# Performance work log

Measured on AMD Instinct MI355X. Metric: run time of the kernel, lower is better.

Reference implementation:

```python
import jax, jax.numpy as jnp
import numpy as np

HIDDEN = 2048
NUM_HEADS = 16
HEAD_DIM = HIDDEN // NUM_HEADS  # 128
SCALE = HEAD_DIM ** -0.5


def setup_inputs() -> dict:
    key = jax.random.key(0)
    ks = jax.random.split(key, 5)
    B, S = 2, 2048
    init = HIDDEN ** -0.5  # roughly kaiming-uniform scale for Linear weights
    return {
        "hidden_states": jax.random.normal(ks[0], (B, S, HIDDEN), dtype=jnp.float32),
        "Wq": jax.random.normal(ks[1], (HIDDEN, HIDDEN), dtype=jnp.float32) * init,
        "Wk": jax.random.normal(ks[2], (HIDDEN, HIDDEN), dtype=jnp.float32) * init,
        "Wv": jax.random.normal(ks[3], (HIDDEN, HIDDEN), dtype=jnp.float32) * init,
        "Wo": jax.random.normal(ks[4], (HIDDEN, HIDDEN), dtype=jnp.float32) * init,
    }


def reference(hidden_states, Wq, Wk, Wv, Wo):
    B, S, _ = hidden_states.shape
    # Projections (nn.Linear: x @ W.T; weights stored as [out, in])
    q = (hidden_states @ Wq.T).reshape(B, S, NUM_HEADS, HEAD_DIM).transpose(0, 2, 1, 3)
    k = (hidden_states @ Wk.T).reshape(B, S, NUM_HEADS, HEAD_DIM).transpose(0, 2, 1, 3)
    v = (hidden_states @ Wv.T).reshape(B, S, NUM_HEADS, HEAD_DIM).transpose(0, 2, 1, 3)
    # Full quadratic attention (faithful to the source's explicit materialization)
    scores = jnp.einsum("bhqd,bhkd->bhqk", q, k) * SCALE  # [B,H,S,S]
    probs = jax.nn.softmax(scores, axis=-1)
    attn = jnp.einsum("bhqk,bhkd->bhqd", probs, v)  # [B,H,S,Dh]
    attn = attn.transpose(0, 2, 1, 3).reshape(B, S, HIDDEN)
    return attn @ Wo.T
```

## Files before the change

kernel.cpp:

```cpp
#include <hip/hip_runtime.h>
#include <cstdint>

#define HIDDEN 2048
#define NHEADS 16
#define DH 128
#define BATCH 2
#define SEQ 2048
#define MTOT 4096
#define BH (BATCH * NHEADS)

typedef __attribute__((ext_vector_type(8))) short bf16x8;
typedef __attribute__((ext_vector_type(4))) float f32x4;

static constexpr float QSCALE = (float)(0.08838834764831845 * 1.4426950408889634);

__device__ __forceinline__ unsigned short f2bf(float f) {
  union { float f; uint32_t u; } v; v.f = f;
  uint32_t r = v.u + 0x7FFFu + ((v.u >> 16) & 1u);
  return (unsigned short)(r >> 16);
}
__device__ __forceinline__ uint32_t cvtpk(float lo, float hi) {
  uint32_t r;
  asm("v_cvt_pk_bf16_f32 %0, %1, %2" : "=v"(r) : "v"(lo), "v"(hi));
  return r;
}
__device__ __forceinline__ f32x4 mfma16(bf16x8 a, bf16x8 b, f32x4 c) {
  return __builtin_amdgcn_mfma_f32_16x16x32_bf16(a, b, c, 0, 0, 0);
}

typedef const __attribute__((address_space(1))) unsigned char* gas1_t;
typedef __attribute__((address_space(3))) unsigned char* las3_t;
__device__ __forceinline__ void gll16(const void* g, void* l) {
  __builtin_amdgcn_global_load_lds((gas1_t)g, (las3_t)l, 16, 0, 0);
}

__global__ __launch_bounds__(256) void cast_all(
    const float* __restrict__ X, const float* __restrict__ Wq,
    const float* __restrict__ Wk, const float* __restrict__ Wv,
    const float* __restrict__ Wo, unsigned short* __restrict__ Xb,
    unsigned short* __restrict__ Wqb, unsigned short* __restrict__ Wkb,
    unsigned short* __restrict__ Wvb, unsigned short* __restrict__ Wob) {
  const int n1 = MTOT * HIDDEN;
  const int i = (blockIdx.x * 256 + threadIdx.x) * 4;
  const float* s;
  unsigned short* d;
  int o;
  if (i < n1) {
    s = X; d = Xb; o = i;
  } else {
    const int j = i - n1;
    const int w = j >> 22;
    o = j & ((1 << 22) - 1);
    s = (w == 0) ? Wq : (w == 1) ? Wk : (w == 2) ? Wv : Wo;
    d = (w == 0) ? Wqb : (w == 1) ? Wkb : (w == 2) ? Wvb : Wob;
  }
  float4 f = *(const float4*)&s[o];
  ushort4 u;
  u.x = f2bf(f.x); u.y = f2bf(f.y); u.z = f2bf(f.z); u.w = f2bf(f.w);
  *(ushort4*)&d[o] = u;
}

template <int VM, bool PF>
__device__ __forceinline__ void pipe_body(
    int kt, char* SM, const unsigned short* aS0, const unsigned short* aS1,
    const unsigned short* bS0, const unsigned short* bS1,
    const unsigned short* bS2, const unsigned short* bS3, int wv, int wr,
    int wc, int g, int lr, f32x4 (&acc)[4][4]) {
  const char* Ac = SM + (kt % 3) * 49152;
  const char* Bc = Ac + 16384;
  char* slot2 = SM + ((kt + 2) % 3) * 49152;
  const size_t ko = (size_t)(kt + 2) * 64;
  const int rx = lr & 7;
  bf16x8 a0[4], b0[4], a1[4], b1[4];
#pragma unroll
  for (int mi = 0; mi < 4; ++mi)
    a0[mi] = *(const bf16x8*)(Ac + (wr * 64 + mi * 16 + lr) * 128 + ((g ^ rx) * 16));
#pragma unroll
  for (int ni = 0; ni < 4; ++ni)
    b0[ni] = *(const bf16x8*)(Bc + (wc * 64 + ni * 16 + lr) * 128 + ((g ^ rx) * 16));
  if (PF) {
    gll16(aS0 + ko, slot2 + wv * 2048);
    gll16(aS1 + ko, slot2 + wv * 2048 + 1024);
    gll16(bS0 + ko, slot2 + 16384 + wv * 4096);
    gll16(bS1 + ko, slot2 + 16384 + wv * 4096 + 1024);
    gll16(bS2 + ko, slot2 + 16384 + wv * 4096 + 2048);
    gll16(bS3 + ko, slot2 + 16384 + wv * 4096 + 3072);
  }
#pragma unroll
  for (int mi = 0; mi < 4; ++mi)
    a1[mi] = *(const bf16x8*)(Ac + (wr * 64 + mi * 16 + lr) * 128 + (((4 + g) ^ rx) * 16));
#pragma unroll
  for (int ni = 0; ni < 4; ++ni)
    b1[ni] = *(const bf16x8*)(Bc + (wc * 64 + ni * 16 + lr) * 128 + (((4 + g) ^ rx) * 16));
  __builtin_amdgcn_s_setprio(1);
#pragma unroll
  for (int mi = 0; mi < 4; ++mi)
#pragma unroll
    for (int ni = 0; ni < 4; ++ni)
      acc[mi][ni] = mfma16(a0[mi], b0[ni], acc[mi][ni]);
#pragma unroll
  for (int mi = 0; mi < 4; ++mi)
#pragma unroll
    for (int ni = 0; ni < 4; ++ni)
      acc[mi][ni] = mfma16(a1[mi], b1[ni], acc[mi][ni]);
  __builtin_amdgcn_s_setprio(0);
  if (VM == 6) asm volatile("s_waitcnt vmcnt(6)" ::: "memory");
  else if (VM == 0) asm volatile("s_waitcnt vmcnt(0)" ::: "memory");
  if (VM >= 0) __builtin_amdgcn_s_barrier();
}

#define PIPE_SETUP(Abase, Bbase)                                              \
  const int idxA0 = wv * 128 + lane, idxA1 = idxA0 + 64;                      \
  const int rA0 = idxA0 >> 3, cA0 = (idxA0 & 7) ^ (rA0 & 7);                  \
  const int rA1 = idxA1 >> 3, cA1 = (idxA1 & 7) ^ (rA1 & 7);                  \
  const unsigned short* aS0 = (Abase) + (size_t)(m0 + rA0) * HIDDEN + cA0 * 8;\
  const unsigned short* aS1 = (Abase) + (size_t)(m0 + rA1) * HIDDEN + cA1 * 8;\
  const int idxB0 = wv * 256 + lane, idxB1 = idxB0 + 64,                      \
            idxB2 = idxB0 + 128, idxB3 = idxB0 + 192;                         \
  const int rB0 = idxB0 >> 3, cB0 = (idxB0 & 7) ^ (rB0 & 7);                  \
  const int rB1 = idxB1 >> 3, cB1 = (idxB1 & 7) ^ (rB1 & 7);                  \
  const int rB2 = idxB2 >> 3, cB2 = (idxB2 & 7) ^ (rB2 & 7);                  \
  const int rB3 = idxB3 >> 3, cB3 = (idxB3 & 7) ^ (rB3 & 7);                  \
  const unsigned short* bS0 = (Bbase) + (size_t)(n0 + rB0) * HIDDEN + cB0 * 8;\
  const unsigned short* bS1 = (Bbase) + (size_t)(n0 + rB1) * HIDDEN + cB1 * 8;\
  const unsigned short* bS2 = (Bbase) + (size_t)(n0 + rB2) * HIDDEN + cB2 * 8;\
  const unsigned short* bS3 = (Bbase) + (size_t)(n0 + rB3) * HIDDEN + cB3 * 8;

#define PIPE_PROLOGUE()                                                       \
  _Pragma("unroll") for (int tt = 0; tt < 2; ++tt) {                          \
    char* slot = SM + tt * 49152;                                             \
    const size_t ko = (size_t)tt * 64;                                        \
    gll16(aS0 + ko, slot + wv * 2048);                                        \
    gll16(aS1 + ko, slot + wv * 2048 + 1024);                                 \
    gll16(bS0 + ko, slot + 16384 + wv * 4096);                                \
    gll16(bS1 + ko, slot + 16384 + wv * 4096 + 1024);                         \
    gll16(bS2 + ko, slot + 16384 + wv * 4096 + 2048);                         \
    gll16(bS3 + ko, slot + 16384 + wv * 4096 + 3072);                         \
  }                                                                           \
  asm volatile("s_waitcnt vmcnt(6)" ::: "memory");                            \
  __builtin_amdgcn_s_barrier();

#define PIPE_LOOP()                                                           \
  for (int kt = 0; kt < 30; ++kt)                                             \
    pipe_body<6, true>(kt, SM, aS0, aS1, bS0, bS1, bS2, bS3, wv, wr, wc, g,   \
                       lr, acc);                                              \
  pipe_body<0, false>(30, SM, aS0, aS1, bS0, bS1, bS2, bS3, wv, wr, wc, g,    \
                      lr, acc);                                               \
  pipe_body<-1, false>(31, SM, aS0, aS1, bS0, bS1, bS2, bS3, wv, wr, wc, g,   \
                       lr, acc);

__global__ __launch_bounds__(512) void gemm_qkv_pipe(
    const unsigned short* __restrict__ A, const unsigned short* __restrict__ Wq,
    const unsigned short* __restrict__ Wk, const unsigned short* __restrict__ Wv,
    unsigned short* __restrict__ Qb, unsigned short* __restrict__ Kb,
    unsigned short* __restrict__ Vb) {
  __shared__ __align__(16) char SM[147456];
  const int tid = threadIdx.x;
  const int lane = tid & 63, wv = tid >> 6;
  const int wr = wv >> 2, wc = wv & 3;
  const int g = lane >> 4, lr = lane & 15;
  const int which = blockIdx.x >> 3;
  const int m0 = blockIdx.y * 128, n0 = (blockIdx.x & 7) * 256;
  const unsigned short* W = (which == 0) ? Wq : (which == 1) ? Wk : Wv;

  PIPE_SETUP(A, W)

  f32x4 acc[4][4];
#pragma unroll
  for (int i = 0; i < 4; ++i)
#pragma unroll
    for (int j = 0; j < 4; ++j) acc[i][j] = (f32x4){0.f, 0.f, 0.f, 0.f};

  PIPE_PROLOGUE()
  PIPE_LOOP()

  const float alpha = (which == 0) ? QSCALE : 1.0f;
  unsigned short* C = (which == 0) ? Qb : (which == 1) ? Kb : Vb;
#pragma unroll
  for (int mi = 0; mi < 4; ++mi)
#pragma unroll
    for (int ni = 0; ni < 4; ++ni)
#pragma unroll
      for (int r = 0; r < 4; ++r) {
        const int row = m0 + wr * 64 + mi * 16 + g * 4 + r;
        const int col = n0 + wc * 64 + ni * 16 + lr;
        const unsigned short v = f2bf(acc[mi][ni][r] * alpha);
        const int b = row >> 11, s = row & (SEQ - 1);
        const int h = col >> 7, d = col & (DH - 1);
        const size_t base = (size_t)(b * NHEADS + h) * SEQ * DH;
        if (which == 0)
          C[base + (size_t)s * DH + d] = v;
        else if (which == 1)
          C[base + (size_t)(s >> 5) * 4096 + (d >> 3) * 256 + (s & 31) * 8 + (d & 7)] = v;
        else
          C[base + (size_t)(s >> 3) * 1024 + d * 8 + (s & 7)] = v;
      }
}

__global__ __launch_bounds__(512) void gemm_out_pipe(
    const unsigned short* __restrict__ A, const unsigned short* __restrict__ W,
    float* __restrict__ C) {
  __shared__ __align__(16) char SM[147456];
  const int tid = threadIdx.x;
  const int lane = tid & 63, wv = tid >> 6;
  const int wr = wv >> 2, wc = wv & 3;
  const int g = lane >> 4, lr = lane & 15;
  const int m0 = blockIdx.y * 128, n0 = blockIdx.x * 256;

  PIPE_SETUP(A, W)

  f32x4 acc[4][4];
#pragma unroll
  for (int i = 0; i < 4; ++i)
#pragma unroll
    for (int j = 0; j < 4; ++j) acc[i][j] = (f32x4){0.f, 0.f, 0.f, 0.f};

  PIPE_PROLOGUE()
  PIPE_LOOP()

#pragma unroll
  for (int mi = 0; mi < 4; ++mi)
#pragma unroll
    for (int ni = 0; ni < 4; ++ni)
#pragma unroll
      for (int r = 0; r < 4; ++r) {
        const int row = m0 + wr * 64 + mi * 16 + g * 4 + r;
        const int col = n0 + wc * 64 + ni * 16 + lr;
        C[(size_t)row * HIDDEN + col] = acc[mi][ni][r];
      }
}

__global__ __launch_bounds__(256, 4) void attn_mfma(const unsigned short* __restrict__ Q,
                                                    const unsigned short* __restrict__ K,
                                                    const unsigned short* __restrict__ V,
                                                    unsigned short* __restrict__ Ab) {
  const int bid = blockIdx.x;
  const int bh = bid & 31;
  const int q0 = (bid >> 5) * 64;
  const int tid = threadIdx.x;
  const int wv = tid >> 6, lane = tid & 63;
  const int g = lane >> 4, lr = lane & 15;
  const unsigned short* Qh = Q + (size_t)bh * SEQ * DH;
  const unsigned short* Kh = K + (size_t)bh * SEQ * DH;
  const unsigned short* Vh = V + (size_t)bh * SEQ * DH;

  __shared__ __align__(16) unsigned short Kls[2][4096];
  __shared__ __align__(16) unsigned short Vls[2][4096];
  __shared__ __align__(16) unsigned short Pw[4][16][40];

  bf16x8 qf[4];
#pragma unroll
  for (int kb = 0; kb < 4; ++kb)
    qf[kb] = *(const bf16x8*)&Qh[(size_t)(q0 + wv * 16 + lr) * DH + kb * 32 + g * 8];

  f32x4 acc[8];
#pragma unroll
  for (int dn = 0; dn < 8; ++dn) acc[dn] = (f32x4){0.f, 0.f, 0.f, 0.f};
  float mrun = -1e30f;
  float lrun = 0.f;

#pragma unroll
  for (int j = 0; j < 2; ++j) {
    const int c = j * 256 + tid;
    gll16(Kh + (size_t)c * 8, (char*)&Kls[0][0] + j * 4096 + wv * 1024);
    gll16(Vh + (size_t)c * 8, (char*)&Vls[0][0] + j * 4096 + wv * 1024);
  }

  for (int t = 0; t < 64; ++t) {
    const int cur = t & 1;
    asm volatile("s_waitcnt vmcnt(0)" ::: "memory");
    __builtin_amdgcn_s_barrier();
    if (t + 1 < 64) {
      const unsigned short* Kn = Kh + (size_t)(t + 1) * 4096;
      const unsigned short* Vn = Vh + (size_t)(t + 1) * 4096;
      char* kd = (char*)&Kls[cur ^ 1][0];
      char* vd = (char*)&Vls[cur ^ 1][0];
#pragma unroll
      for (int j = 0; j < 2; ++j) {
        const int c = j * 256 + tid;
        gll16(Kn + (size_t)c * 8, kd + j * 4096 + wv * 1024);
        gll16(Vn + (size_t)c * 8, vd + j * 4096 + wv * 1024);
      }
    }

    const char* Kc = (const char*)&Kls[cur][0];
    const char* Vc = (const char*)&Vls[cur][0];

    f32x4 st0 = (f32x4){0.f, 0.f, 0.f, 0.f};
    f32x4 st1 = (f32x4){0.f, 0.f, 0.f, 0.f};
    __builtin_amdgcn_s_setprio(1);
#pragma unroll
    for (int kb = 0; kb < 4; ++kb) {
      const int cb = (kb * 4 + g) * 32;
      bf16x8 kf0 = *(const bf16x8*)(Kc + (cb + lr) * 16);
      bf16x8 kf1 = *(const bf16x8*)(Kc + (cb + 16 + lr) * 16);
      st0 = mfma16(kf0, qf[kb], st0);
      st1 = mfma16(kf1, qf[kb], st1);
    }
    __builtin_amdgcn_s_setprio(0);
    float mt = fmaxf(fmaxf(fmaxf(st0[0], st0[1]), fmaxf(st0[2], st0[3])),
                     fmaxf(fmaxf(st1[0], st1[1]), fmaxf(st1[2], st1[3])));
    mt = fmaxf(mt, __shfl_xor(mt, 16));
    mt = fmaxf(mt, __shfl_xor(mt, 32));
    if (!__all(mt <= mrun + 8.0f)) {
      const float mnew = fmaxf(mrun, mt);
      const float corr = __builtin_amdgcn_exp2f(mrun - mnew);
      lrun *= corr;
      mrun = mnew;
      const f32x4 cv = (f32x4){__shfl(corr, g * 4 + 0), __shfl(corr, g * 4 + 1),
                               __shfl(corr, g * 4 + 2), __shfl(corr, g * 4 + 3)};
#pragma unroll
      for (int dn = 0; dn < 8; ++dn) acc[dn] *= cv;
    }
    float p[8], ls = 0.f;
#pragma unroll
    for (int r = 0; r < 4; ++r) {
      p[r] = __builtin_amdgcn_exp2f(st0[r] - mrun);
      p[4 + r] = __builtin_amdgcn_exp2f(st1[r] - mrun);
      ls += p[r] + p[4 + r];
    }
    lrun += ls;
    uint2 pk0, pk1;
    pk0.x = cvtpk(p[0], p[1]); pk0.y = cvtpk(p[2], p[3]);
    pk1.x = cvtpk(p[4], p[5]); pk1.y = cvtpk(p[6], p[7]);
    *(uint2*)&Pw[wv][lr][4 * g] = pk0;
    *(uint2*)&Pw[wv][lr][16 + 4 * g] = pk1;
    bf16x8 ap = *(const bf16x8*)&Pw[wv][lr][8 * g];
    __builtin_amdgcn_s_setprio(1);
#pragma unroll
    for (int dn = 0; dn < 8; ++dn) {
      bf16x8 vf = *(const bf16x8*)(Vc + (g * 128 + dn * 16 + lr) * 16);
      acc[dn] = mfma16(ap, vf, acc[dn]);
    }
    __builtin_amdgcn_s_setprio(0);
  }

  const int b = bh >> 4, h = bh & 15;
  lrun += __shfl_xor(lrun, 16);
  lrun += __shfl_xor(lrun, 32);
  const float inv = 1.f / lrun;
  float ir[4];
#pragma unroll
  for (int r = 0; r < 4; ++r) ir[r] = __shfl(inv, g * 4 + r);
#pragma unroll
  for (int dn = 0; dn < 8; ++dn)
#pragma unroll
    for (int r = 0; r < 4; ++r) {
      const int srow = q0 + wv * 16 + g * 4 + r;
      Ab[((size_t)(b * SEQ + srow) * NHEADS + h) * DH + dn * 16 + lr] =
          f2bf(acc[dn][r] * ir[r]);
    }
}

extern "C" void kernel_launch(void* const* d_in, const int* in_sizes, int n_in,
                              void* d_out, int out_size, void* d_ws,
                              size_t ws_size, hipStream_t stream) {
  const float* X  = (const float*)d_in[0];
  const float* Wq = (const float*)d_in[1];
  const float* Wk = (const float*)d_in[2];
  const float* Wv = (const float*)d_in[3];
  const float* Wo = (const float*)d_in[4];
  float* out = (float*)d_out;

  const int n1 = MTOT * HIDDEN;
  const int n2 = HIDDEN * HIDDEN;

  char* p = (char*)d_ws;
  unsigned short* Xb  = (unsigned short*)(p + 0);
  unsigned short* Qb  = (unsigned short*)(p + 16777216);
  unsigned short* Kb  = (unsigned short*)(p + 33554432);
  unsigned short* Vb  = (unsigned short*)(p + 50331648);
  unsigned short* Wqb = (unsigned short*)(p + 67108864);
  unsigned short* Wkb = (unsigned short*)(p + 75497472);
  unsigned short* Wvb = (unsigned short*)(p + 83886080);
  unsigned short* Wob = (unsigned short*)(p + 92274688);
  unsigned short* Ab  = (unsigned short*)(p + 100663296);

  cast_all<<<(n1 + 4 * n2) / 1024, 256, 0, stream>>>(X, Wq, Wk, Wv, Wo, Xb, Wqb,
                                                     Wkb, Wvb, Wob);

  gemm_qkv_pipe<<<dim3(24, MTOT / 128), 512, 0, stream>>>(Xb, Wqb, Wkb, Wvb,
                                                          Qb, Kb, Vb);

  attn_mfma<<<dim3(1024), 256, 0, stream>>>(Qb, Kb, Vb, Ab);

  gemm_out_pipe<<<dim3(HIDDEN / 256, MTOT / 128), 512, 0, stream>>>(Ab, Wob, out);
}
```

Before: 269.2 us.

## Shrink QKV GEMM tile to 128x128 with 256 threads and double-buffered LDS

The QKV projection GEMM moves from 128x256 tiles with 512 threads and a triple-buffered 144KB LDS pipeline to 128x128 tiles with 256 threads and a 64KB double buffer. The grid doubles to 48x32 blocks, and the smaller LDS footprint may allow more than one block per CU, which should improve occupancy and wave count relative to the CU count. In exchange, each tile reuses global data less, and the loop waits for vmcnt(0) before every iteration, which exposes more load latency. The output GEMM keeps the old pipeline, with its macros inlined.

```diff
diff --git a/kernel.cpp b/kernel.cpp
--- a/kernel.cpp
+++ b/kernel.cpp
@@ -60,110 +60,29 @@
   *(ushort4*)&d[o] = u;
 }
 
-template <int VM, bool PF>
-__device__ __forceinline__ void pipe_body(
-    int kt, char* SM, const unsigned short* aS0, const unsigned short* aS1,
-    const unsigned short* bS0, const unsigned short* bS1,
-    const unsigned short* bS2, const unsigned short* bS3, int wv, int wr,
-    int wc, int g, int lr, f32x4 (&acc)[4][4]) {
-  const char* Ac = SM + (kt % 3) * 49152;
-  const char* Bc = Ac + 16384;
-  char* slot2 = SM + ((kt + 2) % 3) * 49152;
-  const size_t ko = (size_t)(kt + 2) * 64;
-  const int rx = lr & 7;
-  bf16x8 a0[4], b0[4], a1[4], b1[4];
-#pragma unroll
-  for (int mi = 0; mi < 4; ++mi)
-    a0[mi] = *(const bf16x8*)(Ac + (wr * 64 + mi * 16 + lr) * 128 + ((g ^ rx) * 16));
-#pragma unroll
-  for (int ni = 0; ni < 4; ++ni)
-    b0[ni] = *(const bf16x8*)(Bc + (wc * 64 + ni * 16 + lr) * 128 + ((g ^ rx) * 16));
-  if (PF) {
-    gll16(aS0 + ko, slot2 + wv * 2048);
-    gll16(aS1 + ko, slot2 + wv * 2048 + 1024);
-    gll16(bS0 + ko, slot2 + 16384 + wv * 4096);
-    gll16(bS1 + ko, slot2 + 16384 + wv * 4096 + 1024);
-    gll16(bS2 + ko, slot2 + 16384 + wv * 4096 + 2048);
-    gll16(bS3 + ko, slot2 + 16384 + wv * 4096 + 3072);
-  }
-#pragma unroll
-  for (int mi = 0; mi < 4; ++mi)
-    a1[mi] = *(const bf16x8*)(Ac + (wr * 64 + mi * 16 + lr) * 128 + (((4 + g) ^ rx) * 16));
-#pragma unroll
-  for (int ni = 0; ni < 4; ++ni)
-    b1[ni] = *(const bf16x8*)(Bc + (wc * 64 + ni * 16 + lr) * 128 + (((4 + g) ^ rx) * 16));
-  __builtin_amdgcn_s_setprio(1);
-#pragma unroll
-  for (int mi = 0; mi < 4; ++mi)
-#pragma unroll
-    for (int ni = 0; ni < 4; ++ni)
-      acc[mi][ni] = mfma16(a0[mi], b0[ni], acc[mi][ni]);
-#pragma unroll
-  for (int mi = 0; mi < 4; ++mi)
-#pragma unroll
-    for (int ni = 0; ni < 4; ++ni)
-      acc[mi][ni] = mfma16(a1[mi], b1[ni], acc[mi][ni]);
-  __builtin_amdgcn_s_setprio(0);
-  if (VM == 6) asm volatile("s_waitcnt vmcnt(6)" ::: "memory");
-  else if (VM == 0) asm volatile("s_waitcnt vmcnt(0)" ::: "memory");
-  if (VM >= 0) __builtin_amdgcn_s_barrier();
-}
-
-#define PIPE_SETUP(Abase, Bbase)                                              \
-  const int idxA0 = wv * 128 + lane, idxA1 = idxA0 + 64;                      \
-  const int rA0 = idxA0 >> 3, cA0 = (idxA0 & 7) ^ (rA0 & 7);                  \
-  const int rA1 = idxA1 >> 3, cA1 = (idxA1 & 7) ^ (rA1 & 7);                  \
-  const unsigned short* aS0 = (Abase) + (size_t)(m0 + rA0) * HIDDEN + cA0 * 8;\
-  const unsigned short* aS1 = (Abase) + (size_t)(m0 + rA1) * HIDDEN + cA1 * 8;\
-  const int idxB0 = wv * 256 + lane, idxB1 = idxB0 + 64,                      \
-            idxB2 = idxB0 + 128, idxB3 = idxB0 + 192;                         \
-  const int rB0 = idxB0 >> 3, cB0 = (idxB0 & 7) ^ (rB0 & 7);                  \
-  const int rB1 = idxB1 >> 3, cB1 = (idxB1 & 7) ^ (rB1 & 7);                  \
-  const int rB2 = idxB2 >> 3, cB2 = (idxB2 & 7) ^ (rB2 & 7);                  \
-  const int rB3 = idxB3 >> 3, cB3 = (idxB3 & 7) ^ (rB3 & 7);                  \
-  const unsigned short* bS0 = (Bbase) + (size_t)(n0 + rB0) * HIDDEN + cB0 * 8;\
-  const unsigned short* bS1 = (Bbase) + (size_t)(n0 + rB1) * HIDDEN + cB1 * 8;\
-  const unsigned short* bS2 = (Bbase) + (size_t)(n0 + rB2) * HIDDEN + cB2 * 8;\
-  const unsigned short* bS3 = (Bbase) + (size_t)(n0 + rB3) * HIDDEN + cB3 * 8;
-
-#define PIPE_PROLOGUE()                                                       \
-  _Pragma("unroll") for (int tt = 0; tt < 2; ++tt) {                          \
-    char* slot = SM + tt * 49152;                                             \
-    const size_t ko = (size_t)tt * 64;                                        \
-    gll16(aS0 + ko, slot + wv * 2048);                                        \
-    gll16(aS1 + ko, slot + wv * 2048 + 1024);                                 \
-    gll16(bS0 + ko, slot + 16384 + wv * 4096);                                \
-    gll16(bS1 + ko, slot + 16384 + wv * 4096 + 1024);                         \
-    gll16(bS2 + ko, slot + 16384 + wv * 4096 + 2048);                         \
-    gll16(bS3 + ko, slot + 16384 + wv * 4096 + 3072);                         \
-  }                                                                           \
-  asm volatile("s_waitcnt vmcnt(6)" ::: "memory");                            \
-  __builtin_amdgcn_s_barrier();
-
-#define PIPE_LOOP()                                                           \
-  for (int kt = 0; kt < 30; ++kt)                                             \
-    pipe_body<6, true>(kt, SM, aS0, aS1, bS0, bS1, bS2, bS3, wv, wr, wc, g,   \
-                       lr, acc);                                              \
-  pipe_body<0, false>(30, SM, aS0, aS1, bS0, bS1, bS2, bS3, wv, wr, wc, g,    \
-                      lr, acc);                                               \
-  pipe_body<-1, false>(31, SM, aS0, aS1, bS0, bS1, bS2, bS3, wv, wr, wc, g,   \
-                       lr, acc);
-
-__global__ __launch_bounds__(512) void gemm_qkv_pipe(
+__global__ __launch_bounds__(256) void gemm_qkv_pipe(
     const unsigned short* __restrict__ A, const unsigned short* __restrict__ Wq,
     const unsigned short* __restrict__ Wk, const unsigned short* __restrict__ Wv,
     unsigned short* __restrict__ Qb, unsigned short* __restrict__ Kb,
     unsigned short* __restrict__ Vb) {
-  __shared__ __align__(16) char SM[147456];
+  __shared__ __align__(16) char SM[65536];
   const int tid = threadIdx.x;
   const int lane = tid & 63, wv = tid >> 6;
-  const int wr = wv >> 2, wc = wv & 3;
+  const int wr = wv >> 1, wc = wv & 1;
   const int g = lane >> 4, lr = lane & 15;
-  const int which = blockIdx.x >> 3;
-  const int m0 = blockIdx.y * 128, n0 = (blockIdx.x & 7) * 256;
+  const int which = blockIdx.x >> 4;
+  const int m0 = blockIdx.y * 128, n0 = (blockIdx.x & 15) * 128;
   const unsigned short* W = (which == 0) ? Wq : (which == 1) ? Wk : Wv;
 
-  PIPE_SETUP(A, W)
+  const unsigned short* aS[4];
+  const unsigned short* bS[4];
+#pragma unroll
+  for (int j = 0; j < 4; ++j) {
+    const int c = j * 256 + tid;
+    const int row = c >> 3, cc = (c & 7) ^ (row & 7);
+    aS[j] = A + (size_t)(m0 + row) * HIDDEN + cc * 8;
+    bS[j] = W + (size_t)(n0 + row) * HIDDEN + cc * 8;
+  }
 
   f32x4 acc[4][4];
 #pragma unroll
@@ -171,8 +90,52 @@
 #pragma unroll
     for (int j = 0; j < 4; ++j) acc[i][j] = (f32x4){0.f, 0.f, 0.f, 0.f};
 
-  PIPE_PROLOGUE()
-  PIPE_LOOP()
+#pragma unroll
+  for (int j = 0; j < 4; ++j) {
+    gll16(aS[j], SM + j * 4096 + wv * 1024);
+    gll16(bS[j], SM + 16384 + j * 4096 + wv * 1024);
+  }
+
+  const int rx = lr & 7;
+  for (int t = 0; t < 32; ++t) {
+    const char* slot = SM + (t & 1) * 32768;
+    asm volatile("s_waitcnt vmcnt(0)" ::: "memory");
+    __builtin_amdgcn_s_barrier();
+    if (t + 1 < 32) {
+      char* nslot = SM + ((t + 1) & 1) * 32768;
+      const size_t ko = (size_t)(t + 1) * 64;
+#pragma unroll
+      for (int j = 0; j < 4; ++j) {
+        gll16(aS[j] + ko, nslot + j * 4096 + wv * 1024);
+        gll16(bS[j] + ko, nslot + 16384 + j * 4096 + wv * 1024);
+      }
+    }
+    bf16x8 a0[4], b0[4], a1[4], b1[4];
+#pragma unroll
+    for (int mi = 0; mi < 4; ++mi) {
+      const int row = wr * 64 + mi * 16 + lr;
+      a0[mi] = *(const bf16x8*)(slot + row * 128 + ((g ^ rx) * 16));
+      a1[mi] = *(const bf16x8*)(slot + row * 128 + (((4 + g) ^ rx) * 16));
+    }
+#pragma unroll
+    for (int ni = 0; ni < 4; ++ni) {
+      const int row = wc * 64 + ni * 16 + lr;
+      b0[ni] = *(const bf16x8*)(slot + 16384 + row * 128 + ((g ^ rx) * 16));
+      b1[ni] = *(const bf16x8*)(slot + 16384 + row * 128 + (((4 + g) ^ rx) * 16));
+    }
+    __builtin_amdgcn_s_setprio(1);
+#pragma unroll
+    for (int mi = 0; mi < 4; ++mi)
+#pragma unroll
+      for (int ni = 0; ni < 4; ++ni)
+        acc[mi][ni] = mfma16(a0[mi], b0[ni], acc[mi][ni]);
+#pragma unroll
+    for (int mi = 0; mi < 4; ++mi)
+#pragma unroll
+      for (int ni = 0; ni < 4; ++ni)
+        acc[mi][ni] = mfma16(a1[mi], b1[ni], acc[mi][ni]);
+    __builtin_amdgcn_s_setprio(0);
+  }
 
   const float alpha = (which == 0) ? QSCALE : 1.0f;
   unsigned short* C = (which == 0) ? Qb : (which == 1) ? Kb : Vb;
@@ -197,6 +160,55 @@
       }
 }
 
+template <int VM, bool PF>
+__device__ __forceinline__ void pipe_body(
+    int kt, char* SM, const unsigned short* aS0, const unsigned short* aS1,
+    const unsigned short* bS0, const unsigned short* bS1,
+    const unsigned short* bS2, const unsigned short* bS3, int wv, int wr,
+    int wc, int g, int lr, f32x4 (&acc)[4][4]) {
+  const char* Ac = SM + (kt % 3) * 49152;
+  const char* Bc = Ac + 16384;
+  char* slot2 = SM + ((kt + 2) % 3) * 49152;
+  const size_t ko = (size_t)(kt + 2) * 64;
+  const int rx = lr & 7;
+  bf16x8 a0[4], b0[4], a1[4], b1[4];
+#pragma unroll
+  for (int mi = 0; mi < 4; ++mi)
+    a0[mi] = *(const bf16x8*)(Ac + (wr * 64 + mi * 16 + lr) * 128 + ((g ^ rx) * 16));
+#pragma unroll
+  for (int ni = 0; ni < 4; ++ni)
+    b0[ni] = *(const bf16x8*)(Bc + (wc * 64 + ni * 16 + lr) * 128 + ((g ^ rx) * 16));
+  if (PF) {
+    gll16(aS0 + ko, slot2 + wv * 2048);
+    gll16(aS1 + ko, slot2 + wv * 2048 + 1024);
+    gll16(bS0 + ko, slot2 + 16384 + wv * 4096);
+    gll16(bS1 + ko, slot2 + 16384 + wv * 4096 + 1024);
+    gll16(bS2 + ko, slot2 + 16384 + wv * 4096 + 2048);
+    gll16(bS3 + ko, slot2 + 16384 + wv * 4096 + 3072);
+  }
+#pragma unroll
+  for (int mi = 0; mi < 4; ++mi)
+    a1[mi] = *(const bf16x8*)(Ac + (wr * 64 + mi * 16 + lr) * 128 + (((4 + g) ^ rx) * 16));
+#pragma unroll
+  for (int ni = 0; ni < 4; ++ni)
+    b1[ni] = *(const bf16x8*)(Bc + (wc * 64 + ni * 16 + lr) * 128 + (((4 + g) ^ rx) * 16));
+  __builtin_amdgcn_s_setprio(1);
+#pragma unroll
+  for (int mi = 0; mi < 4; ++mi)
+#pragma unroll
+    for (int ni = 0; ni < 4; ++ni)
+      acc[mi][ni] = mfma16(a0[mi], b0[ni], acc[mi][ni]);
+#pragma unroll
+  for (int mi = 0; mi < 4; ++mi)
+#pragma unroll
+    for (int ni = 0; ni < 4; ++ni)
+      acc[mi][ni] = mfma16(a1[mi], b1[ni], acc[mi][ni]);
+  __builtin_amdgcn_s_setprio(0);
+  if (VM == 6) asm volatile("s_waitcnt vmcnt(6)" ::: "memory");
+  else if (VM == 0) asm volatile("s_waitcnt vmcnt(0)" ::: "memory");
+  if (VM >= 0) __builtin_amdgcn_s_barrier();
+}
+
 __global__ __launch_bounds__(512) void gemm_out_pipe(
     const unsigned short* __restrict__ A, const unsigned short* __restrict__ W,
     float* __restrict__ C) {
@@ -207,7 +219,21 @@
   const int g = lane >> 4, lr = lane & 15;
   const int m0 = blockIdx.y * 128, n0 = blockIdx.x * 256;
 
-  PIPE_SETUP(A, W)
+  const int idxA0 = wv * 128 + lane, idxA1 = idxA0 + 64;
+  const int rA0 = idxA0 >> 3, cA0 = (idxA0 & 7) ^ (rA0 & 7);
+  const int rA1 = idxA1 >> 3, cA1 = (idxA1 & 7) ^ (rA1 & 7);
+  const unsigned short* aS0 = A + (size_t)(m0 + rA0) * HIDDEN + cA0 * 8;
+  const unsigned short* aS1 = A + (size_t)(m0 + rA1) * HIDDEN + cA1 * 8;
+  const int idxB0 = wv * 256 + lane, idxB1 = idxB0 + 64,
+            idxB2 = idxB0 + 128, idxB3 = idxB0 + 192;
+  const int rB0 = idxB0 >> 3, cB0 = (idxB0 & 7) ^ (rB0 & 7);
+  const int rB1 = idxB1 >> 3, cB1 = (idxB1 & 7) ^ (rB1 & 7);
+  const int rB2 = idxB2 >> 3, cB2 = (idxB2 & 7) ^ (rB2 & 7);
+  const int rB3 = idxB3 >> 3, cB3 = (idxB3 & 7) ^ (rB3 & 7);
+  const unsigned short* bS0 = W + (size_t)(n0 + rB0) * HIDDEN + cB0 * 8;
+  const unsigned short* bS1 = W + (size_t)(n0 + rB1) * HIDDEN + cB1 * 8;
+  const unsigned short* bS2 = W + (size_t)(n0 + rB2) * HIDDEN + cB2 * 8;
+  const unsigned short* bS3 = W + (size_t)(n0 + rB3) * HIDDEN + cB3 * 8;
 
   f32x4 acc[4][4];
 #pragma unroll
@@ -215,8 +241,27 @@
 #pragma unroll
     for (int j = 0; j < 4; ++j) acc[i][j] = (f32x4){0.f, 0.f, 0.f, 0.f};
 
-  PIPE_PROLOGUE()
-  PIPE_LOOP()
+#pragma unroll
+  for (int tt = 0; tt < 2; ++tt) {
+    char* slot = SM + tt * 49152;
+    const size_t ko = (size_t)tt * 64;
+    gll16(aS0 + ko, slot + wv * 2048);
+    gll16(aS1 + ko, slot + wv * 2048 + 1024);
+    gll16(bS0 + ko, slot + 16384 + wv * 4096);
+    gll16(bS1 + ko, slot + 16384 + wv * 4096 + 1024);
+    gll16(bS2 + ko, slot + 16384 + wv * 4096 + 2048);
+    gll16(bS3 + ko, slot + 16384 + wv * 4096 + 3072);
+  }
+  asm volatile("s_waitcnt vmcnt(6)" ::: "memory");
+  __builtin_amdgcn_s_barrier();
+
+  for (int kt = 0; kt < 30; ++kt)
+    pipe_body<6, true>(kt, SM, aS0, aS1, bS0, bS1, bS2, bS3, wv, wr, wc, g,
+                       lr, acc);
+  pipe_body<0, false>(30, SM, aS0, aS1, bS0, bS1, bS2, bS3, wv, wr, wc, g,
+                      lr, acc);
+  pipe_body<-1, false>(31, SM, aS0, aS1, bS0, bS1, bS2, bS3, wv, wr, wc, g,
+                       lr, acc);
 
 #pragma unroll
   for (int mi = 0; mi < 4; ++mi)
@@ -379,7 +424,7 @@
   cast_all<<<(n1 + 4 * n2) / 1024, 256, 0, stream>>>(X, Wq, Wk, Wv, Wo, Xb, Wqb,
                                                      Wkb, Wvb, Wob);
 
-  gemm_qkv_pipe<<<dim3(24, MTOT / 128), 512, 0, stream>>>(Xb, Wqb, Wkb, Wvb,
+  gemm_qkv_pipe<<<dim3(48, MTOT / 128), 256, 0, stream>>>(Xb, Wqb, Wkb, Wvb,
                                                           Qb, Kb, Vb);
 
   attn_mfma<<<dim3(1024), 256, 0, stream>>>(Qb, Kb, Vb, Ab);
```

After: 285.6 us. +6.1%, slower.
